# Kernel optimization log

Hardware: AMD Instinct MI355X
Metric: run time of the kernel (lower is better)

The kernel has to match this reference:

```python
import jax, jax.numpy as jnp
import numpy as np

DIM = 1024
NUM_HEADS = 8
DIM_HEAD = 64
K_NEIGHBORS = 64
INNER = NUM_HEADS * DIM_HEAD
SCALE = DIM_HEAD ** -0.5


def setup_inputs() -> dict:
    key = jax.random.key(0)
    kx, kq, kk = jax.random.split(key, 3)
    x = jax.random.normal(kx, (2, 2048, DIM), dtype=jnp.float32)
    # nn.Linear(dim, inner_dim, bias=False): weight applied as x @ W.T; store as [dim, inner]
    Wq = jax.random.normal(kq, (DIM, INNER), dtype=jnp.float32) * (DIM ** -0.5)
    Wk = jax.random.normal(kk, (DIM, INNER), dtype=jnp.float32) * (DIM ** -0.5)
    return {"x": x, "Wq": Wq, "Wk": Wk}


def reference(x, Wq, Wk):
    b, n, _ = x.shape
    # project and split heads: (b, n, inner) -> (b, h, n, d)
    q = (x @ Wq).reshape(b, n, NUM_HEADS, DIM_HEAD).transpose(0, 2, 1, 3)
    k = (x @ Wk).reshape(b, n, NUM_HEADS, DIM_HEAD).transpose(0, 2, 1, 3)
    scores = jnp.einsum("bhqd,bhkd->bhqk", q, k) * SCALE
    if K_NEIGHBORS < n:
        top_vals, _ = jax.lax.top_k(scores, K_NEIGHBORS)  # (b,h,n,k)
        min_k = top_vals[..., -1:]  # k-th largest per row
        scores = jnp.where(scores < min_k, -jnp.inf, scores)
    return jax.nn.softmax(scores, axis=-1)
```

## Files before the change

### kernel.cpp

```cpp
#include <hip/hip_runtime.h>
#include <math.h>

#define BATCH 2
#define SEQ   2048
#define DIMIN 1024
#define NHEAD 8
#define DHEAD 64
#define INNER 512
#define KNEI  64
#define SCALE 0.125f
#define GBAND 2e-6f

__global__ __launch_bounds__(256) void proj_kernel(
    const float* __restrict__ x, const float* __restrict__ Wq,
    const float* __restrict__ Wk, float* __restrict__ qk)
{
  const int which = blockIdx.z;
  const float* __restrict__ W = which ? Wk : Wq;
  float* __restrict__ out = qk + (size_t)which * (4096ull * (size_t)INNER);
  const int m0 = blockIdx.y * 64;
  const int n0 = blockIdx.x * 64;
  __shared__ float aT[32][68];
  __shared__ float bS[32][68];
  const int t  = threadIdx.x;
  const int ty = t >> 4, tx = t & 15;
  float acc[4][4] = {};
  for (int k0 = 0; k0 < DIMIN; k0 += 32) {
    {
      const int m = t >> 2, c = t & 3;
      float4 a0 = *(const float4*)(x + (size_t)(m0 + m) * DIMIN + k0 + c * 8);
      float4 a1 = *(const float4*)(x + (size_t)(m0 + m) * DIMIN + k0 + c * 8 + 4);
      aT[c*8+0][m] = a0.x; aT[c*8+1][m] = a0.y;
      aT[c*8+2][m] = a0.z; aT[c*8+3][m] = a0.w;
      aT[c*8+4][m] = a1.x; aT[c*8+5][m] = a1.y;
      aT[c*8+6][m] = a1.z; aT[c*8+7][m] = a1.w;
    }
    {
      const int kk = t >> 6, n = t & 63;
      #pragma unroll
      for (int s5 = 0; s5 < 8; ++s5)
        bS[kk + 4*s5][n] = W[(size_t)(k0 + kk + 4*s5) * INNER + n0 + n];
    }
    __syncthreads();
    #pragma unroll 8
    for (int kk = 0; kk < 32; ++kk) {
      float4 a4 = *(const float4*)&aT[kk][ty*4];
      float4 b4 = *(const float4*)&bS[kk][tx*4];
      float a[4] = {a4.x, a4.y, a4.z, a4.w};
      float b[4] = {b4.x, b4.y, b4.z, b4.w};
      #pragma unroll
      for (int i = 0; i < 4; ++i)
        #pragma unroll
        for (int j = 0; j < 4; ++j)
          acc[i][j] = fmaf(a[i], b[j], acc[i][j]);
    }
    __syncthreads();
  }
  #pragma unroll
  for (int i = 0; i < 4; ++i) {
    float4 v = make_float4(acc[i][0], acc[i][1], acc[i][2], acc[i][3]);
    *(float4*)(out + (size_t)(m0 + ty*4 + i) * INNER + n0 + tx*4) = v;
  }
}

__global__ __launch_bounds__(256) void score_kernel(
    const float* __restrict__ qk, float* __restrict__ out)
{
  const int bh = blockIdx.z;
  const int b  = bh >> 3, h = bh & 7;
  const int m0 = blockIdx.y * 128;
  const int n0 = blockIdx.x * 128;
  const float* __restrict__ q = qk;
  const float* __restrict__ k = qk + 4096ull * (size_t)INNER;
  __shared__ float qT[64][136];
  __shared__ float kT[64][136];
  const int t = threadIdx.x;
  {
    #pragma unroll
    for (int p = 0; p < 2; ++p) {
      const int r  = p*64 + (t >> 2);
      const int d0 = (t & 3) * 16;
      const float* qrow = q + (size_t)(b*SEQ + m0 + r) * INNER + h*DHEAD + d0;
      const float* krow = k + (size_t)(b*SEQ + n0 + r) * INNER + h*DHEAD + d0;
      #pragma unroll
      for (int s = 0; s < 4; ++s) {
        float4 qv = *(const float4*)(qrow + s*4);
        float4 kv = *(const float4*)(krow + s*4);
        qT[d0+s*4+0][r] = qv.x; qT[d0+s*4+1][r] = qv.y;
        qT[d0+s*4+2][r] = qv.z; qT[d0+s*4+3][r] = qv.w;
        kT[d0+s*4+0][r] = kv.x; kT[d0+s*4+1][r] = kv.y;
        kT[d0+s*4+2][r] = kv.z; kT[d0+s*4+3][r] = kv.w;
      }
    }
  }
  __syncthreads();
  const int ty = t >> 4, tx = t & 15;
  float acc[8][8] = {};
  #pragma unroll 2
  for (int kk = 0; kk < 64; ++kk) {
    float4 a0 = *(const float4*)&qT[kk][ty*8];
    float4 a1 = *(const float4*)&qT[kk][ty*8+4];
    float4 b0 = *(const float4*)&kT[kk][tx*8];
    float4 b1 = *(const float4*)&kT[kk][tx*8+4];
    float a[8] = {a0.x,a0.y,a0.z,a0.w,a1.x,a1.y,a1.z,a1.w};
    float bb[8]= {b0.x,b0.y,b0.z,b0.w,b1.x,b1.y,b1.z,b1.w};
    #pragma unroll
    for (int i = 0; i < 8; ++i)
      #pragma unroll
      for (int j = 0; j < 8; ++j)
        acc[i][j] = fmaf(a[i], bb[j], acc[i][j]);
  }
  #pragma unroll
  for (int i = 0; i < 8; ++i) {
    float* orow = out + ((size_t)bh * SEQ + m0 + ty*8 + i) * SEQ + n0 + tx*8;
    float4 v0 = make_float4(acc[i][0]*SCALE, acc[i][1]*SCALE,
                            acc[i][2]*SCALE, acc[i][3]*SCALE);
    float4 v1 = make_float4(acc[i][4]*SCALE, acc[i][5]*SCALE,
                            acc[i][6]*SCALE, acc[i][7]*SCALE);
    *(float4*)(orow)     = v0;
    *(float4*)(orow + 4) = v1;
  }
}

__device__ __forceinline__ unsigned f2key(float f) {
  unsigned u = __float_as_uint(f);
  return (u & 0x80000000u) ? ~u : (u | 0x80000000u);
}
__device__ __forceinline__ float key2f(unsigned kk) {
  unsigned u = (kk & 0x80000000u) ? (kk & 0x7FFFFFFFu) : ~kk;
  return __uint_as_float(u);
}

__global__ __launch_bounds__(256) void topk_softmax_hedge(float* __restrict__ out)
{
  const int wave = threadIdx.x >> 6;
  const int lane = threadIdx.x & 63;
  const size_t row = (size_t)blockIdx.x * 4 + wave;
  float* __restrict__ p = out + row * (size_t)SEQ;

  float s[32];
  #pragma unroll
  for (int i = 0; i < 8; ++i) {
    float4 v = *(const float4*)(p + (size_t)(lane + 64*i) * 4);
    s[i*4+0] = v.x; s[i*4+1] = v.y; s[i*4+2] = v.z; s[i*4+3] = v.w;
  }

  float mx = s[0], mn = s[0];
  #pragma unroll
  for (int i = 1; i < 32; ++i) { mx = fmaxf(mx, s[i]); mn = fminf(mn, s[i]); }
  #pragma unroll
  for (int o = 32; o; o >>= 1) {
    mx = fmaxf(mx, __shfl_xor(mx, o));
    mn = fminf(mn, __shfl_xor(mn, o));
  }

  unsigned lo = f2key(mn);
  unsigned hi = f2key(mx) + 1u;
  while (lo + 1u < hi) {
    const unsigned mid = lo + ((hi - lo) >> 1);
    const float tf = key2f(mid);
    int c = 0;
    #pragma unroll
    for (int i = 0; i < 32; ++i)
      c += __popcll(__ballot(s[i] >= tf));
    if (c >= KNEI) { lo = mid; if (c == KNEI) break; }
    else hi = mid;
  }
  const float thr0 = key2f(lo);

  float mk = 3.4e38f;
  #pragma unroll
  for (int i = 0; i < 32; ++i) mk = (s[i] >= thr0) ? fminf(mk, s[i]) : mk;
  #pragma unroll
  for (int o = 32; o; o >>= 1) mk = fminf(mk, __shfl_xor(mk, o));
  const float s64 = mk;

  int n_hi = 0, n_band = 0;
  #pragma unroll
  for (int i = 0; i < 32; ++i) {
    n_hi   += __popcll(__ballot(s[i] > s64 + GBAND));
    n_band += __popcll(__ballot(fabsf(s[i] - s64) <= GBAND));
  }
  const int r = KNEI - n_hi;
  const bool amb = (n_band != r);
  float fb = (float)r / (float)max(n_band, 1);
  fb = fminf(fmaxf(fb, 0.f), 1.f);

  float z = 0.f;
  #pragma unroll
  for (int i = 0; i < 32; ++i) {
    float f;
    if (amb) {
      f = (s[i] > s64 + GBAND) ? 1.f
        : ((fabsf(s[i] - s64) <= GBAND) ? fb : 0.f);
    } else {
      f = (s[i] >= s64) ? 1.f : 0.f;
    }
    float ex = f * __expf(s[i] - mx);
    s[i] = ex; z += ex;
  }
  #pragma unroll
  for (int o = 32; o; o >>= 1) z += __shfl_xor(z, o);
  const float rz = 1.0f / z;

  #pragma unroll
  for (int i = 0; i < 8; ++i) {
    float4 v = make_float4(s[i*4+0]*rz, s[i*4+1]*rz, s[i*4+2]*rz, s[i*4+3]*rz);
    *(float4*)(p + (size_t)(lane + 64*i) * 4) = v;
  }
}

extern "C" void kernel_launch(void* const* d_in, const int* in_sizes, int n_in,
                              void* d_out, int out_size, void* d_ws, size_t ws_size,
                              hipStream_t stream) {
  const float* x  = (const float*)d_in[0];
  const float* Wq = (const float*)d_in[1];
  const float* Wk = (const float*)d_in[2];
  float* out = (float*)d_out;
  float* ws  = (float*)d_ws;

  proj_kernel<<<dim3(INNER/64, (BATCH*SEQ)/64, 2), 256, 0, stream>>>(x, Wq, Wk, ws);
  score_kernel<<<dim3(SEQ/128, SEQ/128, BATCH*NHEAD), 256, 0, stream>>>(ws, out);
  topk_softmax_hedge<<<dim3((BATCH*NHEAD*SEQ)/4), 256, 0, stream>>>(out);
}
```

Baseline: 361.0 us.

## Enlarge projection GEMM tiles, reverse top-k row order, use nontemporal stores

The projection GEMM moves from 64x64 tiles with a 4x4 per-thread micro-tile to 128x128 tiles with an 8x8 micro-tile, and the W tile is now loaded with vectorized float4 copies. This raises arithmetic intensity and cuts global loads, but the grid shrinks to 256 blocks and register pressure rises. The top-k softmax kernel walks rows in reverse, so it starts on the most recently written score rows that may still sit in cache. Its final writes use nontemporal stores to avoid polluting the cache.

```diff
diff --git a/kernel.cpp b/kernel.cpp
--- a/kernel.cpp
+++ b/kernel.cpp
@@ -11,6 +11,8 @@
 #define SCALE 0.125f
 #define GBAND 2e-6f
 
+typedef float v4f __attribute__((ext_vector_type(4)));
+
 __global__ __launch_bounds__(256) void proj_kernel(
     const float* __restrict__ x, const float* __restrict__ Wq,
     const float* __restrict__ Wk, float* __restrict__ qk)
@@ -18,48 +20,53 @@
   const int which = blockIdx.z;
   const float* __restrict__ W = which ? Wk : Wq;
   float* __restrict__ out = qk + (size_t)which * (4096ull * (size_t)INNER);
-  const int m0 = blockIdx.y * 64;
-  const int n0 = blockIdx.x * 64;
-  __shared__ float aT[32][68];
-  __shared__ float bS[32][68];
+  const int m0 = blockIdx.y * 128;
+  const int n0 = blockIdx.x * 128;
+  __shared__ float aT[32][132];
+  __shared__ float bS[32][132];
   const int t  = threadIdx.x;
   const int ty = t >> 4, tx = t & 15;
-  float acc[4][4] = {};
+  float acc[8][8] = {};
   for (int k0 = 0; k0 < DIMIN; k0 += 32) {
     {
-      const int m = t >> 2, c = t & 3;
-      float4 a0 = *(const float4*)(x + (size_t)(m0 + m) * DIMIN + k0 + c * 8);
-      float4 a1 = *(const float4*)(x + (size_t)(m0 + m) * DIMIN + k0 + c * 8 + 4);
-      aT[c*8+0][m] = a0.x; aT[c*8+1][m] = a0.y;
-      aT[c*8+2][m] = a0.z; aT[c*8+3][m] = a0.w;
-      aT[c*8+4][m] = a1.x; aT[c*8+5][m] = a1.y;
-      aT[c*8+6][m] = a1.z; aT[c*8+7][m] = a1.w;
+      const int m = t >> 1, c = (t & 1) * 16;
+      const float* xr = x + (size_t)(m0 + m) * DIMIN + k0 + c;
+      #pragma unroll
+      for (int s5 = 0; s5 < 4; ++s5) {
+        float4 v = *(const float4*)(xr + s5*4);
+        aT[c+s5*4+0][m] = v.x; aT[c+s5*4+1][m] = v.y;
+        aT[c+s5*4+2][m] = v.z; aT[c+s5*4+3][m] = v.w;
+      }
     }
     {
-      const int kk = t >> 6, n = t & 63;
-      #pragma unroll
-      for (int s5 = 0; s5 < 8; ++s5)
-        bS[kk + 4*s5][n] = W[(size_t)(k0 + kk + 4*s5) * INNER + n0 + n];
+      const int kk = t >> 3, n = (t & 7) * 16;
+      const float* wr = W + (size_t)(k0 + kk) * INNER + n0 + n;
+      #pragma unroll
+      for (int s5 = 0; s5 < 4; ++s5)
+        *(float4*)&bS[kk][n + s5*4] = *(const float4*)(wr + s5*4);
     }
     __syncthreads();
-    #pragma unroll 8
+    #pragma unroll 4
     for (int kk = 0; kk < 32; ++kk) {
-      float4 a4 = *(const float4*)&aT[kk][ty*4];
-      float4 b4 = *(const float4*)&bS[kk][tx*4];
-      float a[4] = {a4.x, a4.y, a4.z, a4.w};
-      float b[4] = {b4.x, b4.y, b4.z, b4.w};
-      #pragma unroll
-      for (int i = 0; i < 4; ++i)
+      float4 a0 = *(const float4*)&aT[kk][ty*8];
+      float4 a1 = *(const float4*)&aT[kk][ty*8+4];
+      float4 b0 = *(const float4*)&bS[kk][tx*8];
+      float4 b1 = *(const float4*)&bS[kk][tx*8+4];
+      float a[8] = {a0.x,a0.y,a0.z,a0.w,a1.x,a1.y,a1.z,a1.w};
+      float b[8] = {b0.x,b0.y,b0.z,b0.w,b1.x,b1.y,b1.z,b1.w};
+      #pragma unroll
+      for (int i = 0; i < 8; ++i)
         #pragma unroll
-        for (int j = 0; j < 4; ++j)
+        for (int j = 0; j < 8; ++j)
           acc[i][j] = fmaf(a[i], b[j], acc[i][j]);
     }
     __syncthreads();
   }
   #pragma unroll
-  for (int i = 0; i < 4; ++i) {
-    float4 v = make_float4(acc[i][0], acc[i][1], acc[i][2], acc[i][3]);
-    *(float4*)(out + (size_t)(m0 + ty*4 + i) * INNER + n0 + tx*4) = v;
+  for (int i = 0; i < 8; ++i) {
+    float* orow = out + (size_t)(m0 + ty*8 + i) * INNER + n0 + tx*8;
+    *(float4*)(orow)     = make_float4(acc[i][0], acc[i][1], acc[i][2], acc[i][3]);
+    *(float4*)(orow + 4) = make_float4(acc[i][4], acc[i][5], acc[i][6], acc[i][7]);
   }
 }
 
@@ -113,12 +120,10 @@
   #pragma unroll
   for (int i = 0; i < 8; ++i) {
     float* orow = out + ((size_t)bh * SEQ + m0 + ty*8 + i) * SEQ + n0 + tx*8;
-    float4 v0 = make_float4(acc[i][0]*SCALE, acc[i][1]*SCALE,
-                            acc[i][2]*SCALE, acc[i][3]*SCALE);
-    float4 v1 = make_float4(acc[i][4]*SCALE, acc[i][5]*SCALE,
-                            acc[i][6]*SCALE, acc[i][7]*SCALE);
-    *(float4*)(orow)     = v0;
-    *(float4*)(orow + 4) = v1;
+    *(float4*)(orow)     = make_float4(acc[i][0]*SCALE, acc[i][1]*SCALE,
+                                       acc[i][2]*SCALE, acc[i][3]*SCALE);
+    *(float4*)(orow + 4) = make_float4(acc[i][4]*SCALE, acc[i][5]*SCALE,
+                                       acc[i][6]*SCALE, acc[i][7]*SCALE);
   }
 }
 
@@ -135,7 +140,7 @@
 {
   const int wave = threadIdx.x >> 6;
   const int lane = threadIdx.x & 63;
-  const size_t row = (size_t)blockIdx.x * 4 + wave;
+  const size_t row = (size_t)(gridDim.x - 1 - blockIdx.x) * 4 + wave;
   float* __restrict__ p = out + row * (size_t)SEQ;
 
   float s[32];
@@ -205,8 +210,8 @@
 
   #pragma unroll
   for (int i = 0; i < 8; ++i) {
-    float4 v = make_float4(s[i*4+0]*rz, s[i*4+1]*rz, s[i*4+2]*rz, s[i*4+3]*rz);
-    *(float4*)(p + (size_t)(lane + 64*i) * 4) = v;
+    v4f v = { s[i*4+0]*rz, s[i*4+1]*rz, s[i*4+2]*rz, s[i*4+3]*rz };
+    __builtin_nontemporal_store(v, (v4f*)(p + (size_t)(lane + 64*i) * 4));
   }
 }
 
@@ -219,7 +224,7 @@
   float* out = (float*)d_out;
   float* ws  = (float*)d_ws;
 
-  proj_kernel<<<dim3(INNER/64, (BATCH*SEQ)/64, 2), 256, 0, stream>>>(x, Wq, Wk, ws);
+  proj_kernel<<<dim3(INNER/128, (BATCH*SEQ)/128, 2), 256, 0, stream>>>(x, Wq, Wk, ws);
   score_kernel<<<dim3(SEQ/128, SEQ/128, BATCH*NHEAD), 256, 0, stream>>>(ws, out);
   topk_softmax_hedge<<<dim3((BATCH*NHEAD*SEQ)/4), 256, 0, stream>>>(out);
 }
```

Result: no change. 365.4 us (+1.2%).
